# Kernel optimization log

Hardware: AMD Instinct MI355X
Metric: run time of the kernel (lower is better)

Reference implementation:

```python
import jax, jax.numpy as jnp
import numpy as np

SLOPE = 0.2  # LeakyReLU negative slope
EPS = 1e-8


def setup_inputs() -> dict:
    key = jax.random.key(0)
    ks = jax.random.split(key, 10)
    B, LL, D, H = 16, 257, 64, 128
    in_dim = D + 1  # lags=1 -> lags*D + 1
    sc = 0.1
    return {
        "x": jax.random.normal(ks[0], (B, LL, D), dtype=jnp.float32),
        "W1": jax.random.normal(ks[1], (D, H, in_dim), dtype=jnp.float32) * sc,
        "b1": jax.random.normal(ks[2], (D, H), dtype=jnp.float32) * sc,
        "W2": jax.random.normal(ks[3], (D, H, H), dtype=jnp.float32) * sc,
        "b2": jax.random.normal(ks[4], (D, H), dtype=jnp.float32) * sc,
        "W3": jax.random.normal(ks[5], (D, H, H), dtype=jnp.float32) * sc,
        "b3": jax.random.normal(ks[6], (D, H), dtype=jnp.float32) * sc,
        "W4": jax.random.normal(ks[7], (D, 1, H), dtype=jnp.float32) * sc,
        "b4": jax.random.normal(ks[8], (D, 1), dtype=jnp.float32) * sc,
        "lags": 1,
    }


def _forward(x, W1, b1, W2, b2, W3, b3, W4, b4, lags):
    B, LL, D = x.shape
    length = LL - lags
    # sliding windows of size lags+1 along time: [B, length, lags+1, D]
    windows = jnp.stack([x[:, i:i + length] for i in range(lags + 1)], axis=2)
    N = B * length
    x_lags = windows[:, :, :-1].reshape(N, lags * D)  # [N, lags*D]
    x_t = windows[:, :, -1].reshape(N, D)             # [N, D]

    def per_latent(w1, bb1, w2, bb2, w3, bb3, w4, bb4, xti):
        inp = jnp.concatenate([x_lags, xti[:, None]], axis=-1)  # [N, lags*D+1]
        p1 = inp @ w1.T + bb1
        s1 = jnp.where(p1 > 0, 1.0, SLOPE)
        a1 = p1 * s1
        p2 = a1 @ w2.T + bb2
        s2 = jnp.where(p2 > 0, 1.0, SLOPE)
        a2 = p2 * s2
        p3 = a2 @ w3.T + bb3
        s3 = jnp.where(p3 > 0, 1.0, SLOPE)
        a3 = p3 * s3
        out = a3 @ w4.T + bb4  # [N, 1]
        # analytic d out / d x_{t,i} (Jacobian diagonal): chain through LeakyReLU slopes
        d = s1 * w1[:, -1]      # [N, H]
        d = s2 * (d @ w2.T)     # [N, H]
        d = s3 * (d @ w3.T)     # [N, H]
        deriv = d @ w4[0]       # [N]
        return out[:, 0], deriv

    res, deriv = jax.vmap(per_latent, in_axes=(0, 0, 0, 0, 0, 0, 0, 0, 1))(
        W1, b1, W2, b2, W3, b3, W4, b4, x_t)  # res, deriv: [D, N]
    residuals = res.T.reshape(B, length, D)
    log_abs_det = jnp.log(jnp.abs(deriv) + EPS).sum(axis=0).reshape(B, length)
    return residuals, log_abs_det


def reference(x, W1, b1, W2, b2, W3, b3, W4, b4, lags):
    return _forward(x, W1, b1, W2, b2, W3, b3, W4, b4, lags)
```

## Files before the change

kernel.cpp:

```cpp
#include <hip/hip_runtime.h>
#include <hip/hip_bf16.h>
#include <math.h>

typedef _Float16 f16;
typedef _Float16 f16x8 __attribute__((ext_vector_type(8)));
typedef _Float16 f16x4 __attribute__((ext_vector_type(4)));
typedef float f32x4 __attribute__((ext_vector_type(4)));

#define MFMA(a, b, c) __builtin_amdgcn_mfma_f32_16x16x32_f16((a), (b), (c), 0, 0, 0)

constexpr int Dd = 64;
constexpr int Hh = 128;
constexpr int Nn = 4096;
constexpr int NT = 32;
constexpr float SLP = 0.2f;
constexpr float INV2K = 1.0f / 2048.0f;

constexpr int PD = 81920;
constexpr size_t W1L_OFF = (size_t)Dd * PD * 2;
constexpr size_t WS_NEEDED = W1L_OFF + (size_t)Dd * Hh * 4;

__device__ __forceinline__ int swz(int r, int c) {
  return (r << 7) + ((((c >> 3) ^ (r & 15)) << 3) | (c & 7));
}
__device__ __forceinline__ int swzK64(int r, int c) {
  return (r << 6) + (((((c >> 3) ^ r) & 7) << 3) | (c & 7));
}
__device__ __forceinline__ int swzF(int n, int h) {
  return (n << 7) + ((((h >> 2) ^ n) & 31) << 2) + (h & 3);
}

struct HL { f16 h, l; };
__device__ __forceinline__ HL split(float v) {
  HL r;
  r.h = (f16)v;
  r.l = (f16)((v - (float)r.h) * 2048.0f);
  return r;
}

__device__ __forceinline__ void cp_lds_async512(const void* g, void* l, int nbytes, int tid) {
  const int lane = tid & 63, wv = tid >> 6;
  for (int base = wv * 1024; base < nbytes; base += 8192) {
    __builtin_amdgcn_global_load_lds(
        (const __attribute__((address_space(1))) void*)((const char*)g + base + lane * 16),
        (__attribute__((address_space(3))) void*)((char*)l + base), 16, 0, 0);
  }
}

__global__ __launch_bounds__(256)
void prep_kernel(const float* __restrict__ W1, const float* __restrict__ W2,
                 const float* __restrict__ W3, f16* __restrict__ wsf,
                 float* __restrict__ w1lg, float* __restrict__ out_log) {
  const int gid = blockIdx.x * 256 + threadIdx.x;
  if (gid < Dd * Hh) w1lg[gid] = W1[(gid >> 7) * 8320 + (gid & 127) * 65 + 64];
  if (gid < Nn) out_log[gid] = 0.f;

  const int d = gid / 10240;
  const int r = gid - d * 10240;
  f16* outd = wsf + (size_t)d * PD;
  float vv[8];
  f16* dst;
  int plane;
  if (r < 2048) {
    int rem = r & 1023;
    int hf = r >> 10;
    plane = rem >> 9;
    int j = rem & 511;
    int row = j >> 3, sc = j & 7;
    int h = hf * 64 + row;
    int k0 = (sc ^ (row & 7)) << 3;
    const float* src = W1 + d * 8320 + h * 65 + k0;
#pragma unroll
    for (int e = 0; e < 8; e++) vv[e] = src[e];
    dst = outd + r * 8;
  } else {
    int r2 = r - 2048;
    int wmat = r2 >> 12;
    int rr4 = r2 & 4095;
    int chunk = rr4 >> 10;
    int rr = rr4 & 1023;
    plane = rr >> 9;
    int j = rr & 511;
    int row = j >> 4, sc = j & 15;
    int k0 = (sc ^ (row & 15)) << 3;
    const float* srcb = (wmat == 0 ? W2 : W3) + d * 16384;
    const float* src = srcb + (chunk * 32 + row) * 128 + k0;
    float4 v0 = *(const float4*)src, v1 = *(const float4*)(src + 4);
    vv[0] = v0.x; vv[1] = v0.y; vv[2] = v0.z; vv[3] = v0.w;
    vv[4] = v1.x; vv[5] = v1.y; vv[6] = v1.z; vv[7] = v1.w;
    dst = outd + 16384 + wmat * 32768 + chunk * 8192 + rr * 8;
  }
  if (plane) {
#pragma unroll
    for (int e = 0; e < 8; e++) {
      f16 hi = (f16)vv[e];
      vv[e] = (vv[e] - (float)hi) * 2048.0f;
    }
  }
  f16x8 o;
#pragma unroll
  for (int e = 0; e < 8; e++) o[e] = (f16)vv[e];
  *(f16x8*)dst = o;
}

__device__ __forceinline__ void mid_chunk(const f16* ws,
                                          const f16x8* axh, const f16x8* axl,
                                          const f16x8* ayh, const f16x8* ayl,
                                          int hrc, int quad,
                                          f32x4& aP, f32x4& aS, f32x4& dP, f32x4& dS) {
#pragma unroll
  for (int kc = 0; kc < 4; kc++) {
    int ko = kc * 32 + quad * 8;
    f16x8 wh = *(const f16x8*)&ws[swz(hrc, ko)];
    f16x8 wl = *(const f16x8*)&ws[4096 + swz(hrc, ko)];
    aP = MFMA(wh, axh[kc], aP);
    aS = MFMA(wl, axh[kc], aS);
    aS = MFMA(wh, axl[kc], aS);
    dP = MFMA(wh, ayh[kc], dP);
    dS = MFMA(wl, ayh[kc], dS);
    dS = MFMA(wh, ayl[kc], dS);
  }
}

__global__ __launch_bounds__(512, 4)
void np_prior_v2(const float* __restrict__ x, const f16* __restrict__ wsw,
                 const float* __restrict__ w1lg,
                 const float* __restrict__ b1, const float* __restrict__ b2,
                 const float* __restrict__ b3, const float* __restrict__ W4,
                 const float* __restrict__ b4,
                 float* __restrict__ out_res, float* __restrict__ out_log) {
  extern __shared__ char dsm[];
  f16* AH = (f16*)dsm;
  f16* AL = AH + 8192;
  f16* DH = AL + 8192;
  f16* DL = DH + 8192;
  f16* Ws = (f16*)(dsm + 65536);
  float* A3F = (float*)dsm;
  float* D3F = (float*)(dsm + 32768);

  const int tid = threadIdx.x, d = blockIdx.y, n0 = blockIdx.x * 64;
  const int lane = tid & 63, wv = tid >> 6, l15 = lane & 15, quad = lane >> 4;
  const int nt = wv & 3, wq = wv >> 2;
  const int ra = nt * 16 + l15;
  const int hrc = wq * 16 + l15;

  const f16* wd = wsw + (size_t)d * PD;
  const float* w1l = w1lg + d * Hh;
  const float* b1d = b1 + d * Hh;
  const f32x4 zero = {0.f, 0.f, 0.f, 0.f};

  cp_lds_async512(wd, Ws, 16384, tid);
  {
    int n = tid >> 3, k8 = (tid & 7) << 3;
    int ng = n0 + n, bb = ng >> 8, tt = ng & 255;
    const float* xs = &x[(bb * 257 + tt) * 64 + k8];
    float4 v0 = *(const float4*)xs, v1 = *(const float4*)(xs + 4);
    float va[8] = {v0.x, v0.y, v0.z, v0.w, v1.x, v1.y, v1.z, v1.w};
    f16x8 vh, vl;
#pragma unroll
    for (int e = 0; e < 8; e++) {
      HL s = split(va[e]);
      vh[e] = s.h; vl[e] = s.l;
    }
    int o = swz(n, k8);
    *(f16x8*)&AH[o] = vh;
    *(f16x8*)&AL[o] = vl;
  }
  float xtv;
  {
    int ng = n0 + ra, bb = ng >> 8, tt = ng & 255;
    xtv = x[(bb * 257 + tt + 1) * 64 + d];
  }
  __syncthreads();

  f16x8 l1xh[2], l1xl[2];
#pragma unroll
  for (int kc = 0; kc < 2; kc++) {
    int ko = kc * 32 + quad * 8;
    l1xh[kc] = *(const f16x8*)&AH[swz(ra, ko)];
    l1xl[kc] = *(const f16x8*)&AL[swz(ra, ko)];
  }
#pragma unroll 1
  for (int cf = 0; cf < 2; cf++) {
    f32x4 P[2], S[2];
#pragma unroll
    for (int hf2 = 0; hf2 < 2; hf2++) {
      int hr64 = hf2 * 32 + hrc;
      P[hf2] = zero; S[hf2] = zero;
#pragma unroll
      for (int kc = 0; kc < 2; kc++) {
        int ko = kc * 32 + quad * 8;
        f16x8 wh = *(const f16x8*)&Ws[swzK64(hr64, ko)];
        f16x8 wl = *(const f16x8*)&Ws[4096 + swzK64(hr64, ko)];
        P[hf2] = MFMA(wh, l1xh[kc], P[hf2]);
        S[hf2] = MFMA(wl, l1xh[kc], S[hf2]);
        S[hf2] = MFMA(wh, l1xl[kc], S[hf2]);
      }
    }
    __syncthreads();
    cp_lds_async512(wd + (cf == 0 ? 8192 : 16384), Ws, 16384, tid);
#pragma unroll
    for (int hf2 = 0; hf2 < 2; hf2++) {
      int hb = cf * 64 + hf2 * 32 + wq * 16 + quad * 4;
      float4 wv4 = *(const float4*)&w1l[hb];
      float4 bv4 = *(const float4*)&b1d[hb];
      f16x4 ah, al, dh, dl;
#pragma unroll
      for (int j = 0; j < 4; j++) {
        float w1j = (&wv4.x)[j];
        float p = P[hf2][j] + S[hf2][j] * INV2K + xtv * w1j + (&bv4.x)[j];
        float s = p > 0.f ? 1.f : SLP;
        HL av = split(p * s), dv = split(s * w1j);
        ah[j] = av.h; al[j] = av.l; dh[j] = dv.h; dl[j] = dv.l;
      }
      int o = swz(ra, hb);
      *(f16x4*)&AH[o] = ah; *(f16x4*)&AL[o] = al;
      *(f16x4*)&DH[o] = dh; *(f16x4*)&DL[o] = dl;
    }
    __syncthreads();
  }

  {
    f16x8 axh[4], axl[4], ayh[4], ayl[4];
#pragma unroll
    for (int kc = 0; kc < 4; kc++) {
      int ko = kc * 32 + quad * 8;
      axh[kc] = *(const f16x8*)&AH[swz(ra, ko)];
      axl[kc] = *(const f16x8*)&AL[swz(ra, ko)];
      ayh[kc] = *(const f16x8*)&DH[swz(ra, ko)];
      ayl[kc] = *(const f16x8*)&DL[swz(ra, ko)];
    }
    __syncthreads();
    const float* b2d = b2 + d * Hh;
#pragma unroll 1
    for (int c = 0; c < 4; c++) {
      if (c > 0) {
        __syncthreads();
        cp_lds_async512(wd + 16384 + c * 8192, Ws, 16384, tid);
        __syncthreads();
      }
      f32x4 aP = zero, aS = zero, dP = zero, dS = zero;
      mid_chunk(Ws, axh, axl, ayh, ayl, hrc, quad, aP, aS, dP, dS);
      {
        int hb = c * 32 + wq * 16 + quad * 4;
        float4 bv4 = *(const float4*)&b2d[hb];
        f16x4 ah, al, dh, dl;
#pragma unroll
        for (int j = 0; j < 4; j++) {
          float p = aP[j] + aS[j] * INV2K + (&bv4.x)[j];
          float s = p > 0.f ? 1.f : SLP;
          float dd = s * (dP[j] + dS[j] * INV2K);
          HL av = split(p * s), dv = split(dd);
          ah[j] = av.h; al[j] = av.l; dh[j] = dv.h; dl[j] = dv.l;
        }
        int o = swz(ra, hb);
        *(f16x4*)&AH[o] = ah; *(f16x4*)&AL[o] = al;
        *(f16x4*)&DH[o] = dh; *(f16x4*)&DL[o] = dl;
      }
    }
  }
  __syncthreads();
  cp_lds_async512(wd + 49152, Ws, 16384, tid);

  {
    f16x8 axh[4], axl[4], ayh[4], ayl[4];
#pragma unroll
    for (int kc = 0; kc < 4; kc++) {
      int ko = kc * 32 + quad * 8;
      axh[kc] = *(const f16x8*)&AH[swz(ra, ko)];
      axl[kc] = *(const f16x8*)&AL[swz(ra, ko)];
      ayh[kc] = *(const f16x8*)&DH[swz(ra, ko)];
      ayl[kc] = *(const f16x8*)&DL[swz(ra, ko)];
    }
    __syncthreads();
    const float* b3d = b3 + d * Hh;
#pragma unroll 1
    for (int c = 0; c < 4; c++) {
      if (c > 0) {
        __syncthreads();
        cp_lds_async512(wd + 49152 + c * 8192, Ws, 16384, tid);
        __syncthreads();
      }
      f32x4 aP = zero, aS = zero, dP = zero, dS = zero;
      mid_chunk(Ws, axh, axl, ayh, ayl, hrc, quad, aP, aS, dP, dS);
      {
        int hb = c * 32 + wq * 16 + quad * 4;
        float4 bv4 = *(const float4*)&b3d[hb];
        float4 pa, pd;
#pragma unroll
        for (int j = 0; j < 4; j++) {
          float p = aP[j] + aS[j] * INV2K + (&bv4.x)[j];
          float s = p > 0.f ? 1.f : SLP;
          (&pa.x)[j] = p * s;
          (&pd.x)[j] = s * (dP[j] + dS[j] * INV2K);
        }
        *(float4*)&A3F[swzF(ra, hb)] = pa;
        *(float4*)&D3F[swzF(ra, hb)] = pd;
      }
    }
  }
  __syncthreads();

  {
    int n = tid >> 3, oct = tid & 7;
    const float* w4d = W4 + d * Hh;
    float sr = 0.f, sd = 0.f;
#pragma unroll
    for (int i = 0; i < 4; i++) {
      int c = oct * 16 + i * 4;
      float4 va = *(const float4*)&A3F[swzF(n, c)];
      float4 vd = *(const float4*)&D3F[swzF(n, c)];
      float4 w = *(const float4*)&w4d[c];
      sr += va.x * w.x + va.y * w.y + va.z * w.z + va.w * w.w;
      sd += vd.x * w.x + vd.y * w.y + vd.z * w.z + vd.w * w.w;
    }
    sr += __shfl_xor(sr, 1); sr += __shfl_xor(sr, 2); sr += __shfl_xor(sr, 4);
    sd += __shfl_xor(sd, 1); sd += __shfl_xor(sd, 2); sd += __shfl_xor(sd, 4);
    if (oct == 0) {
      int ng = n0 + n;
      out_res[ng * 64 + d] = sr + b4[d];
      atomicAdd(&out_log[ng], logf(fabsf(sd) + 1e-8f));
    }
  }
}

__device__ __forceinline__ void stage_wf(f16* WH, f16* WL,
                                         const float* __restrict__ g, int tid) {
  for (int i = tid; i < 2048; i += 256) {
    int h = i >> 5, k4 = (i & 31) << 2;
    float4 v = ((const float4*)g)[i];
    HL a = split(v.x), b = split(v.y), c = split(v.z), e = split(v.w);
    int o = swz(h, k4);
    *(f16x4*)&WH[o] = f16x4{a.h, b.h, c.h, e.h};
    *(f16x4*)&WL[o] = f16x4{a.l, b.l, c.l, e.l};
  }
}

__device__ __forceinline__ void mid_mfma_half(
    const f16* AH, const f16* AL, const f16* DH, const f16* DL,
    const f16* WH, const f16* WL, int nt, int wq, int l15, int quad,
    f32x4* aP, f32x4* aS, f32x4* dP, f32x4* dS) {
#pragma unroll
  for (int kc = 0; kc < 4; kc++) {
    int ko = kc * 32 + quad * 8;
    int ra = nt * 16 + l15;
    f16x8 xh = *(const f16x8*)&AH[swz(ra, ko)];
    f16x8 xl = *(const f16x8*)&AL[swz(ra, ko)];
    f16x8 yh = *(const f16x8*)&DH[swz(ra, ko)];
    f16x8 yl = *(const f16x8*)&DL[swz(ra, ko)];
#pragma unroll
    for (int c2 = 0; c2 < 2; c2++) {
      int hr = (2 * wq + c2) * 16 + l15;
      f16x8 wh = *(const f16x8*)&WH[swz(hr, ko)];
      f16x8 wl = *(const f16x8*)&WL[swz(hr, ko)];
      aP[c2] = MFMA(wh, xh, aP[c2]);
      aS[c2] = MFMA(wl, xh, aS[c2]);
      aS[c2] = MFMA(wh, xl, aS[c2]);
      dP[c2] = MFMA(wh, yh, dP[c2]);
      dS[c2] = MFMA(wl, yh, dS[c2]);
      dS[c2] = MFMA(wh, yl, dS[c2]);
    }
  }
}

__global__ __launch_bounds__(256, 2)
void np_prior_fb(const float* __restrict__ x,
                 const float* __restrict__ W1, const float* __restrict__ b1,
                 const float* __restrict__ W2, const float* __restrict__ b2,
                 const float* __restrict__ W3, const float* __restrict__ b3,
                 const float* __restrict__ W4, const float* __restrict__ b4,
                 float* __restrict__ out_res, float* __restrict__ out_log) {
  __shared__ float4 smem[4096];
  f16* AH = (f16*)smem;
  f16* AL = AH + NT * 128;
  f16* DH = AL + NT * 128;
  f16* DL = DH + NT * 128;
  f16* WHp = (f16*)((char*)smem + 32768);
  f16* WLp = WHp + 64 * 128;
  float* A3F = (float*)smem;
  float* D3F = (float*)((char*)smem + 16384);

  const int tid = threadIdx.x, d = blockIdx.y, n0 = blockIdx.x * NT;
  const int lane = tid & 63, wv = tid >> 6, l15 = lane & 15, quad = lane >> 4;
  const int nt = wv & 1, wq = wv >> 1;

  const float* W1d = W1 + d * Hh * 65;
  const float* b1d = b1 + d * Hh;
  const f32x4 zero = {0.f, 0.f, 0.f, 0.f};

  for (int i = tid; i < NT * 16; i += 256) {
    int n = i >> 4, k4 = (i & 15) << 2;
    int ng = n0 + n, bb = ng >> 8, tt = ng & 255;
    float4 v = *(const float4*)&x[(bb * 257 + tt) * 64 + k4];
    HL a = split(v.x), b = split(v.y), c = split(v.z), e = split(v.w);
    int o = swz(n, k4);
    *(f16x4*)&AH[o] = f16x4{a.h, b.h, c.h, e.h};
    *(f16x4*)&AL[o] = f16x4{a.l, b.l, c.l, e.l};
  }
  float xtv;
  {
    int ng = n0 + nt * 16 + l15, bb = ng >> 8, tt = ng & 255;
    xtv = x[(bb * 257 + tt + 1) * 64 + d];
  }
  for (int i = tid; i < 64 * 64; i += 256) {
    int h = i >> 6, k = i & 63;
    HL s = split(W1d[h * 65 + k]);
    int o = swz(h, k);
    WHp[o] = s.h; WLp[o] = s.l;
  }
  __syncthreads();

  f32x4 l1P[2][2], l1S[2][2];
  for (int hf = 0; hf < 2; hf++) {
    if (hf == 1) {
      __syncthreads();
      for (int i = tid; i < 64 * 64; i += 256) {
        int h = i >> 6, k = i & 63;
        HL s = split(W1d[(64 + h) * 65 + k]);
        int o = swz(h, k);
        WHp[o] = s.h; WLp[o] = s.l;
      }
      __syncthreads();
    }
    l1P[hf][0] = zero; l1P[hf][1] = zero;
    l1S[hf][0] = zero; l1S[hf][1] = zero;
#pragma unroll
    for (int kc = 0; kc < 2; kc++) {
      int ko = kc * 32 + quad * 8;
      f16x8 xh = *(const f16x8*)&AH[swz(nt * 16 + l15, ko)];
      f16x8 xl = *(const f16x8*)&AL[swz(nt * 16 + l15, ko)];
#pragma unroll
      for (int c2 = 0; c2 < 2; c2++) {
        int hr = (2 * wq + c2) * 16 + l15;
        f16x8 wh = *(const f16x8*)&WHp[swz(hr, ko)];
        f16x8 wl = *(const f16x8*)&WLp[swz(hr, ko)];
        l1P[hf][c2] = MFMA(wh, xh, l1P[hf][c2]);
        l1S[hf][c2] = MFMA(wl, xh, l1S[hf][c2]);
        l1S[hf][c2] = MFMA(wh, xl, l1S[hf][c2]);
      }
    }
  }
  __syncthreads();

  {
    int n = nt * 16 + l15;
#pragma unroll
    for (int hf = 0; hf < 2; hf++)
#pragma unroll
      for (int c2 = 0; c2 < 2; c2++) {
        int hb = hf * 64 + (2 * wq + c2) * 16 + quad * 4;
        f16x4 ah, al, dh, dl;
#pragma unroll
        for (int j = 0; j < 4; j++) {
          int h = hb + j;
          float w1j = W1d[h * 65 + 64];
          float p = l1P[hf][c2][j] + l1S[hf][c2][j] * INV2K + xtv * w1j + b1d[h];
          float s = p > 0.f ? 1.f : SLP;
          HL av = split(p * s), dv = split(s * w1j);
          ah[j] = av.h; al[j] = av.l; dh[j] = dv.h; dl[j] = dv.l;
        }
        int o = swz(n, hb);
        *(f16x4*)&AH[o] = ah; *(f16x4*)&AL[o] = al;
        *(f16x4*)&DH[o] = dh; *(f16x4*)&DL[o] = dl;
      }
  }
  stage_wf(WHp, WLp, W2 + d * Hh * Hh, tid);
  __syncthreads();

  f32x4 aP[2][2], aS[2][2], dP[2][2], dS[2][2];
  for (int hf = 0; hf < 2; hf++) {
    if (hf == 1) {
      __syncthreads();
      stage_wf(WHp, WLp, W2 + d * Hh * Hh + 64 * 128, tid);
      __syncthreads();
    }
    aP[hf][0] = zero; aP[hf][1] = zero; aS[hf][0] = zero; aS[hf][1] = zero;
    dP[hf][0] = zero; dP[hf][1] = zero; dS[hf][0] = zero; dS[hf][1] = zero;
    mid_mfma_half(AH, AL, DH, DL, WHp, WLp, nt, wq, l15, quad,
                  aP[hf], aS[hf], dP[hf], dS[hf]);
  }
  __syncthreads();

  {
    const float* b2d = b2 + d * Hh;
    int n = nt * 16 + l15;
#pragma unroll
    for (int hf = 0; hf < 2; hf++)
#pragma unroll
      for (int c2 = 0; c2 < 2; c2++) {
        int hb = hf * 64 + (2 * wq + c2) * 16 + quad * 4;
        f16x4 ah, al, dh, dl;
#pragma unroll
        for (int j = 0; j < 4; j++) {
          int h = hb + j;
          float p = aP[hf][c2][j] + aS[hf][c2][j] * INV2K + b2d[h];
          float s = p > 0.f ? 1.f : SLP;
          float dd = s * (dP[hf][c2][j] + dS[hf][c2][j] * INV2K);
          HL av = split(p * s), dv = split(dd);
          ah[j] = av.h; al[j] = av.l; dh[j] = dv.h; dl[j] = dv.l;
        }
        int o = swz(n, hb);
        *(f16x4*)&AH[o] = ah; *(f16x4*)&AL[o] = al;
        *(f16x4*)&DH[o] = dh; *(f16x4*)&DL[o] = dl;
      }
  }
  stage_wf(WHp, WLp, W3 + d * Hh * Hh, tid);
  __syncthreads();

  for (int hf = 0; hf < 2; hf++) {
    if (hf == 1) {
      __syncthreads();
      stage_wf(WHp, WLp, W3 + d * Hh * Hh + 64 * 128, tid);
      __syncthreads();
    }
    aP[hf][0] = zero; aP[hf][1] = zero; aS[hf][0] = zero; aS[hf][1] = zero;
    dP[hf][0] = zero; dP[hf][1] = zero; dS[hf][0] = zero; dS[hf][1] = zero;
    mid_mfma_half(AH, AL, DH, DL, WHp, WLp, nt, wq, l15, quad,
                  aP[hf], aS[hf], dP[hf], dS[hf]);
  }
  __syncthreads();

  {
    const float* b3d = b3 + d * Hh;
    int n = nt * 16 + l15;
#pragma unroll
    for (int hf = 0; hf < 2; hf++)
#pragma unroll
      for (int c2 = 0; c2 < 2; c2++) {
        int hb = hf * 64 + (2 * wq + c2) * 16 + quad * 4;
        float4 pa, pd;
#pragma unroll
        for (int j = 0; j < 4; j++) {
          int h = hb + j;
          float p = aP[hf][c2][j] + aS[hf][c2][j] * INV2K + b3d[h];
          float s = p > 0.f ? 1.f : SLP;
          (&pa.x)[j] = p * s;
          (&pd.x)[j] = s * (dP[hf][c2][j] + dS[hf][c2][j] * INV2K);
        }
        *(float4*)&A3F[swzF(n, hb)] = pa;
        *(float4*)&D3F[swzF(n, hb)] = pd;
      }
  }
  __syncthreads();

  {
    int n = tid >> 3, oct = tid & 7;
    const float* w4d = W4 + d * Hh;
    float sr = 0.f, sd = 0.f;
#pragma unroll
    for (int i = 0; i < 4; i++) {
      int c = oct * 16 + i * 4;
      float4 va = *(const float4*)&A3F[swzF(n, c)];
      float4 vd = *(const float4*)&D3F[swzF(n, c)];
      float4 w = *(const float4*)&w4d[c];
      sr += va.x * w.x + va.y * w.y + va.z * w.z + va.w * w.w;
      sd += vd.x * w.x + vd.y * w.y + vd.z * w.z + vd.w * w.w;
    }
    sr += __shfl_xor(sr, 1); sr += __shfl_xor(sr, 2); sr += __shfl_xor(sr, 4);
    sd += __shfl_xor(sd, 1); sd += __shfl_xor(sd, 2); sd += __shfl_xor(sd, 4);
    if (oct == 0) {
      int ng = n0 + n;
      out_res[ng * 64 + d] = sr + b4[d];
      atomicAdd(&out_log[ng], logf(fabsf(sd) + 1e-8f));
    }
  }
}

extern "C" void kernel_launch(void* const* d_in, const int* in_sizes, int n_in,
                              void* d_out, int out_size, void* d_ws, size_t ws_size,
                              hipStream_t stream) {
  (void)in_sizes; (void)n_in; (void)out_size;
  const float* x  = (const float*)d_in[0];
  const float* W1 = (const float*)d_in[1];
  const float* b1 = (const float*)d_in[2];
  const float* W2 = (const float*)d_in[3];
  const float* b2 = (const float*)d_in[4];
  const float* W3 = (const float*)d_in[5];
  const float* b3 = (const float*)d_in[6];
  const float* W4 = (const float*)d_in[7];
  const float* b4 = (const float*)d_in[8];

  float* out_res = (float*)d_out;
  float* out_log = out_res + Nn * Dd;

  static int big_lds = -1;
  if (big_lds < 0) {
    big_lds = (hipFuncSetAttribute(
                   (const void*)np_prior_v2,
                   hipFuncAttributeMaxDynamicSharedMemorySize, 81920) ==
               hipSuccess)
                  ? 1
                  : 0;
  }

  if (ws_size >= WS_NEEDED && big_lds == 1) {
    f16* wsf = (f16*)d_ws;
    float* w1lg = (float*)((char*)d_ws + W1L_OFF);
    prep_kernel<<<2560, 256, 0, stream>>>(W1, W2, W3, wsf, w1lg, out_log);
    dim3 grid(Nn / 64, Dd);
    np_prior_v2<<<grid, 512, 81920, stream>>>(x, wsf, w1lg, b1, b2, b3, W4,
                                              b4, out_res, out_log);
  } else {
    hipMemsetAsync(out_log, 0, Nn * sizeof(float), stream);
    dim3 grid(Nn / NT, Dd);
    np_prior_fb<<<grid, 256, 0, stream>>>(x, W1, b1, W2, b2, W3, b3, W4, b4,
                                          out_res, out_log);
  }
}
```

Measured before the change: 212.2 us.

## Prefetch layer-2/3 weight chunks into freed activation LDS to cut barriers

Once the activation fragments sit in registers, the layer 2 and 3 weight chunks are loaded into the now-free activation LDS region as well as the weight buffer. This allows several chunks to be in flight at once instead of running a serial load-sync-compute loop per chunk. New activations are kept in registers and written back after all chunks finish, so the buffers being read are not overwritten early. This removes several barriers and exposed global-to-LDS latency per layer, at the cost of more live registers and careful buffer-aliasing ordering.

```diff
diff --git a/kernel.cpp b/kernel.cpp
--- a/kernel.cpp
+++ b/kernel.cpp
@@ -122,8 +122,53 @@
   }
 }
 
+__device__ __forceinline__ void l2chunk(const f16* wbase, int hb,
+                                        const f16x8* axh, const f16x8* axl,
+                                        const f16x8* ayh, const f16x8* ayl,
+                                        int hrc, int quad, int ra,
+                                        const float* bd, f16* DHp, f16* DLp,
+                                        f16x4& ahO, f16x4& alO) {
+  const f32x4 zero = {0.f, 0.f, 0.f, 0.f};
+  f32x4 aP = zero, aS = zero, dP = zero, dS = zero;
+  mid_chunk(wbase, axh, axl, ayh, ayl, hrc, quad, aP, aS, dP, dS);
+  float4 bv4 = *(const float4*)&bd[hb];
+  f16x4 dh, dl;
+#pragma unroll
+  for (int j = 0; j < 4; j++) {
+    float p = aP[j] + aS[j] * INV2K + (&bv4.x)[j];
+    float s = p > 0.f ? 1.f : SLP;
+    float dd = s * (dP[j] + dS[j] * INV2K);
+    HL av = split(p * s), dv = split(dd);
+    ahO[j] = av.h; alO[j] = av.l; dh[j] = dv.h; dl[j] = dv.l;
+  }
+  int o = swz(ra, hb);
+  *(f16x4*)&DHp[o] = dh;
+  *(f16x4*)&DLp[o] = dl;
+}
+
+__device__ __forceinline__ void l3chunk(const f16* wbase, int hb,
+                                        const f16x8* axh, const f16x8* axl,
+                                        const f16x8* ayh, const f16x8* ayl,
+                                        int hrc, int quad, int ra,
+                                        const float* bd, float* D3Fp,
+                                        float4& paO) {
+  const f32x4 zero = {0.f, 0.f, 0.f, 0.f};
+  f32x4 aP = zero, aS = zero, dP = zero, dS = zero;
+  mid_chunk(wbase, axh, axl, ayh, ayl, hrc, quad, aP, aS, dP, dS);
+  float4 bv4 = *(const float4*)&bd[hb];
+  float4 pd;
+#pragma unroll
+  for (int j = 0; j < 4; j++) {
+    float p = aP[j] + aS[j] * INV2K + (&bv4.x)[j];
+    float s = p > 0.f ? 1.f : SLP;
+    (&paO.x)[j] = p * s;
+    (&pd.x)[j] = s * (dP[j] + dS[j] * INV2K);
+  }
+  *(float4*)&D3Fp[swzF(ra, hb)] = pd;
+}
+
 __global__ __launch_bounds__(512, 4)
-void np_prior_v2(const float* __restrict__ x, const f16* __restrict__ wsw,
+void np_prior_v3(const float* __restrict__ x, const f16* __restrict__ wsw,
                  const float* __restrict__ w1lg,
                  const float* __restrict__ b1, const float* __restrict__ b2,
                  const float* __restrict__ b3, const float* __restrict__ W4,
@@ -231,36 +276,29 @@
       ayl[kc] = *(const f16x8*)&DL[swz(ra, ko)];
     }
     __syncthreads();
+    cp_lds_async512(wd + 24576, dsm, 16384, tid);
+    cp_lds_async512(wd + 32768, dsm + 16384, 16384, tid);
     const float* b2d = b2 + d * Hh;
-#pragma unroll 1
-    for (int c = 0; c < 4; c++) {
-      if (c > 0) {
-        __syncthreads();
-        cp_lds_async512(wd + 16384 + c * 8192, Ws, 16384, tid);
-        __syncthreads();
-      }
-      f32x4 aP = zero, aS = zero, dP = zero, dS = zero;
-      mid_chunk(Ws, axh, axl, ayh, ayl, hrc, quad, aP, aS, dP, dS);
-      {
-        int hb = c * 32 + wq * 16 + quad * 4;
-        float4 bv4 = *(const float4*)&b2d[hb];
-        f16x4 ah, al, dh, dl;
-#pragma unroll
-        for (int j = 0; j < 4; j++) {
-          float p = aP[j] + aS[j] * INV2K + (&bv4.x)[j];
-          float s = p > 0.f ? 1.f : SLP;
-          float dd = s * (dP[j] + dS[j] * INV2K);
-          HL av = split(p * s), dv = split(dd);
-          ah[j] = av.h; al[j] = av.l; dh[j] = dv.h; dl[j] = dv.l;
-        }
-        int o = swz(ra, hb);
-        *(f16x4*)&AH[o] = ah; *(f16x4*)&AL[o] = al;
-        *(f16x4*)&DH[o] = dh; *(f16x4*)&DL[o] = dl;
-      }
-    }
-  }
-  __syncthreads();
-  cp_lds_async512(wd + 49152, Ws, 16384, tid);
+    const int hb0 = wq * 16 + quad * 4;
+    f16x4 ah0, al0, ah1, al1, ah2, al2, ah3, al3;
+    l2chunk(Ws, hb0, axh, axl, ayh, ayl, hrc, quad, ra, b2d, DH, DL, ah0, al0);
+    __syncthreads();
+    cp_lds_async512(wd + 40960, Ws, 16384, tid);
+    l2chunk((const f16*)dsm, hb0 + 32, axh, axl, ayh, ayl, hrc, quad, ra,
+            b2d, DH, DL, ah1, al1);
+    l2chunk((const f16*)(dsm + 16384), hb0 + 64, axh, axl, ayh, ayl, hrc,
+            quad, ra, b2d, DH, DL, ah2, al2);
+    __syncthreads();
+    l2chunk(Ws, hb0 + 96, axh, axl, ayh, ayl, hrc, quad, ra, b2d, DH, DL,
+            ah3, al3);
+    __syncthreads();
+    cp_lds_async512(wd + 49152, Ws, 16384, tid);
+    *(f16x4*)&AH[swz(ra, hb0)] = ah0;      *(f16x4*)&AL[swz(ra, hb0)] = al0;
+    *(f16x4*)&AH[swz(ra, hb0 + 32)] = ah1; *(f16x4*)&AL[swz(ra, hb0 + 32)] = al1;
+    *(f16x4*)&AH[swz(ra, hb0 + 64)] = ah2; *(f16x4*)&AL[swz(ra, hb0 + 64)] = al2;
+    *(f16x4*)&AH[swz(ra, hb0 + 96)] = ah3; *(f16x4*)&AL[swz(ra, hb0 + 96)] = al3;
+    __syncthreads();
+  }
 
   {
     f16x8 axh[4], axl[4], ayh[4], ayl[4];
@@ -273,33 +311,27 @@
       ayl[kc] = *(const f16x8*)&DL[swz(ra, ko)];
     }
     __syncthreads();
+    cp_lds_async512(wd + 57344, dsm, 16384, tid);
+    cp_lds_async512(wd + 65536, dsm + 16384, 16384, tid);
     const float* b3d = b3 + d * Hh;
-#pragma unroll 1
-    for (int c = 0; c < 4; c++) {
-      if (c > 0) {
-        __syncthreads();
-        cp_lds_async512(wd + 49152 + c * 8192, Ws, 16384, tid);
-        __syncthreads();
-      }
-      f32x4 aP = zero, aS = zero, dP = zero, dS = zero;
-      mid_chunk(Ws, axh, axl, ayh, ayl, hrc, quad, aP, aS, dP, dS);
-      {
-        int hb = c * 32 + wq * 16 + quad * 4;
-        float4 bv4 = *(const float4*)&b3d[hb];
-        float4 pa, pd;
-#pragma unroll
-        for (int j = 0; j < 4; j++) {
-          float p = aP[j] + aS[j] * INV2K + (&bv4.x)[j];
-          float s = p > 0.f ? 1.f : SLP;
-          (&pa.x)[j] = p * s;
-          (&pd.x)[j] = s * (dP[j] + dS[j] * INV2K);
-        }
-        *(float4*)&A3F[swzF(ra, hb)] = pa;
-        *(float4*)&D3F[swzF(ra, hb)] = pd;
-      }
-    }
-  }
-  __syncthreads();
+    const int hb0 = wq * 16 + quad * 4;
+    float4 pa0, pa1, pa2, pa3;
+    l3chunk(Ws, hb0, axh, axl, ayh, ayl, hrc, quad, ra, b3d, D3F, pa0);
+    __syncthreads();
+    cp_lds_async512(wd + 73728, Ws, 16384, tid);
+    l3chunk((const f16*)dsm, hb0 + 32, axh, axl, ayh, ayl, hrc, quad, ra,
+            b3d, D3F, pa1);
+    l3chunk((const f16*)(dsm + 16384), hb0 + 64, axh, axl, ayh, ayl, hrc,
+            quad, ra, b3d, D3F, pa2);
+    __syncthreads();
+    l3chunk(Ws, hb0 + 96, axh, axl, ayh, ayl, hrc, quad, ra, b3d, D3F, pa3);
+    __syncthreads();
+    *(float4*)&A3F[swzF(ra, hb0)] = pa0;
+    *(float4*)&A3F[swzF(ra, hb0 + 32)] = pa1;
+    *(float4*)&A3F[swzF(ra, hb0 + 64)] = pa2;
+    *(float4*)&A3F[swzF(ra, hb0 + 96)] = pa3;
+    __syncthreads();
+  }
 
   {
     int n = tid >> 3, oct = tid & 7;
@@ -586,7 +618,7 @@
   static int big_lds = -1;
   if (big_lds < 0) {
     big_lds = (hipFuncSetAttribute(
-                   (const void*)np_prior_v2,
+                   (const void*)np_prior_v3,
                    hipFuncAttributeMaxDynamicSharedMemorySize, 81920) ==
                hipSuccess)
                   ? 1
@@ -598,7 +630,7 @@
     float* w1lg = (float*)((char*)d_ws + W1L_OFF);
     prep_kernel<<<2560, 256, 0, stream>>>(W1, W2, W3, wsf, w1lg, out_log);
     dim3 grid(Nn / 64, Dd);
-    np_prior_v2<<<grid, 512, 81920, stream>>>(x, wsf, w1lg, b1, b2, b3, W4,
+    np_prior_v3<<<grid, 512, 81920, stream>>>(x, wsf, w1lg, b1, b2, b3, W4,
                                               b4, out_res, out_log);
   } else {
     hipMemsetAsync(out_log, 0, Nn * sizeof(float), stream);
```

Result: slower. 222.6 us (+4.9%).
